# Kernel optimization log

Measured on AMD Instinct MI355X. Metric: run time of the kernel, lower is better.

The kernel has to match this reference:

```python
import jax, jax.numpy as jnp
import numpy as np


def setup_inputs() -> dict:
    key = jax.random.key(0)
    k1, k2 = jax.random.split(key)
    tensor_1 = jax.random.normal(k1, (8192, 256), dtype=jnp.float32)
    tensor_2 = jax.random.normal(k2, (16384, 256), dtype=jnp.float32)
    return {"tensor_1": tensor_1, "tensor_2": tensor_2}


def reference(tensor_1, tensor_2):
    # L2-normalize along the feature dim (matches torch .norm(dim=-1), no eps)
    n1 = tensor_1 / jnp.linalg.norm(tensor_1, axis=-1, keepdims=True)  # [N, d]
    n2 = tensor_2 / jnp.linalg.norm(tensor_2, axis=-1, keepdims=True)  # [M, d]
    cos_sim = jnp.einsum("nd,md->nm", n1, n2)  # [N, M] cosine similarity
    top3, _ = jax.lax.top_k(cos_sim, 3)        # [N, 3]
    return top3.mean(axis=-1)                  # [N]
```

## Files before the change

### kernel.cpp

```cpp
#include <hip/hip_runtime.h>
#include <hip/hip_bf16.h>
#include <stdint.h>

#define N1 8192
#define N2 16384
#define DIM 256
#define NSPLIT 16
#define BM 128
#define BN 128
#define BK 128
#define COLS_PER_SPLIT (N2 / NSPLIT)
#define NT_PER_SPLIT (COLS_PER_SPLIT / BN)
#define NPART (NSPLIT * 2)

typedef short v8s  __attribute__((ext_vector_type(8)));
typedef float f32x4 __attribute__((ext_vector_type(4)));

#define GLD16(g, l)                                                                         \
  __builtin_amdgcn_global_load_lds((const __attribute__((address_space(1))) uint32_t*)(g),  \
                                   (__attribute__((address_space(3))) uint32_t*)(l), 16, 0, 0)

__device__ __forceinline__ void top3_insert(float v, float& t0, float& t1, float& t2) {
    float nt1 = __builtin_amdgcn_fmed3f(v, t0, t1);
    float nt2 = __builtin_amdgcn_fmed3f(v, t1, t2);
    t0 = fmaxf(t0, v);
    t1 = nt1;
    t2 = nt2;
}

__global__ __launch_bounds__(256) void normalize_kernel(
        const float* __restrict__ inA, const float* __restrict__ inB,
        __hip_bfloat16* __restrict__ outA, __hip_bfloat16* __restrict__ outB) {
    const int gw   = blockIdx.x * 4 + (threadIdx.x >> 6);
    const int lane = threadIdx.x & 63;
    const float* in;
    __hip_bfloat16* out;
    int row;
    if (gw < N1) { in = inA; out = outA; row = gw; }
    else         { in = inB; out = outB; row = gw - N1; }
    const float4 v = *(const float4*)(in + (size_t)row * DIM + lane * 4);
    float s = v.x * v.x + v.y * v.y + v.z * v.z + v.w * v.w;
    #pragma unroll
    for (int off = 32; off; off >>= 1) s += __shfl_xor(s, off, 64);
    const float inv = 1.0f / sqrtf(s);
    __hip_bfloat16 o[4];
    o[0] = __float2bfloat16(v.x * inv);
    o[1] = __float2bfloat16(v.y * inv);
    o[2] = __float2bfloat16(v.z * inv);
    o[3] = __float2bfloat16(v.w * inv);
    *(uint2*)(out + (size_t)row * DIM + lane * 4) = *(uint2*)o;
}

__global__ __launch_bounds__(256, 2) void gemm_top3_kernel(
        const __hip_bfloat16* __restrict__ A, const __hip_bfloat16* __restrict__ B,
        float* __restrict__ partial) {
    __shared__ char smem[32768 + 32768];
    char* tileA = smem;
    char* tileB = smem + 32768;

    const int tid  = threadIdx.x;
    const int wave = tid >> 6;
    const int lane = tid & 63;
    const int lo   = lane & 15;
    const int quad = lane >> 4;
    const int rb    = blockIdx.x >> 4;
    const int split = blockIdx.x & 15;
    const int row0 = rb * BM;
    const int C0   = split * COLS_PER_SPLIT;
    const int wr = (wave >> 1) * 64;
    const int wc = (wave & 1) * 64;

    const int lr  = lane >> 4;
    const int s16 = lane & 15;

    const char* Agbase = (const char*)A + ((size_t)(row0 + wave * 32 + lr)) * 512;
    const char* Bgbase = (const char*)B + ((size_t)(C0   + wave * 32 + lr)) * 512;
    char* AldsBase = tileA + wave * 32 * 256;
    char* BldsBase = tileB + wave * 32 * 256;

    int aoff[4], boff[4];
    #pragma unroll
    for (int ks = 0; ks < 4; ks++) {
        const int swz = ((ks * 4 + quad) ^ lo) * 16;
        aoff[ks] = (wr + lo) * 256 + swz;
        boff[ks] = (wc + lo) * 256 + swz;
    }

    float t0[16], t1[16], t2[16];
    #pragma unroll
    for (int i = 0; i < 16; i++) { t0[i] = -1e30f; t1[i] = -1e30f; t2[i] = -1e30f; }

    for (int nt = 0; nt < NT_PER_SPLIT; ++nt) {
        f32x4 acc[4][4];
        #pragma unroll
        for (int kk = 0; kk < 2; kk++) {
            __syncthreads();
            #pragma unroll
            for (int j = 0; j < 8; j++) {
                const int sxj = (s16 ^ ((j * 4 + lr) & 15)) * 16;
                GLD16(Agbase + (size_t)j * 2048 + kk * 256 + sxj, AldsBase + j * 1024);
                GLD16(Bgbase + (size_t)nt * 65536 + (size_t)j * 2048 + kk * 256 + sxj,
                      BldsBase + j * 1024);
            }
            __syncthreads();
            #pragma unroll
            for (int ks = 0; ks < 4; ks++) {
                v8s af[4];
                #pragma unroll
                for (int rt = 0; rt < 4; rt++)
                    af[rt] = *(const v8s*)(tileA + aoff[ks] + rt * 4096);
                #pragma unroll
                for (int ct = 0; ct < 4; ct++) {
                    v8s bf = *(const v8s*)(tileB + boff[ks] + ct * 4096);
                    #pragma unroll
                    for (int rt = 0; rt < 4; rt++) {
                        if (kk == 0 && ks == 0)
                            acc[rt][ct] = __builtin_amdgcn_mfma_f32_16x16x32_bf16(
                                af[rt], bf, (f32x4){0.f, 0.f, 0.f, 0.f}, 0, 0, 0);
                        else
                            acc[rt][ct] = __builtin_amdgcn_mfma_f32_16x16x32_bf16(
                                af[rt], bf, acc[rt][ct], 0, 0, 0);
                    }
                }
            }
        }
        #pragma unroll
        for (int rt = 0; rt < 4; rt++)
            #pragma unroll
            for (int r = 0; r < 4; r++) {
                const int i = rt * 4 + r;
                #pragma unroll
                for (int ct = 0; ct < 4; ct++)
                    top3_insert(acc[rt][ct][r], t0[i], t1[i], t2[i]);
            }
    }

    #pragma unroll
    for (int step = 1; step < 16; step <<= 1) {
        #pragma unroll
        for (int i = 0; i < 16; i++) {
            float b0 = __shfl_xor(t0[i], step, 64);
            float b1 = __shfl_xor(t1[i], step, 64);
            float b2 = __shfl_xor(t2[i], step, 64);
            top3_insert(b0, t0[i], t1[i], t2[i]);
            top3_insert(b1, t0[i], t1[i], t2[i]);
            top3_insert(b2, t0[i], t1[i], t2[i]);
        }
    }

    if (lo == 0) {
        #pragma unroll
        for (int rt = 0; rt < 4; rt++)
            #pragma unroll
            for (int r = 0; r < 4; r++) {
                const int i = rt * 4 + r;
                const int row = row0 + wr + rt * 16 + quad * 4 + r;
                float* p = partial + ((size_t)row * NPART + (split * 2 + (wave & 1))) * 3;
                p[0] = t0[i]; p[1] = t1[i]; p[2] = t2[i];
            }
    }
}

__global__ __launch_bounds__(256) void merge_kernel(
        const float* __restrict__ partial, float* __restrict__ out) {
    const int row = blockIdx.x * 256 + threadIdx.x;
    if (row >= N1) return;
    const float* p = partial + (size_t)row * NPART * 3;
    float t0 = -1e30f, t1 = -1e30f, t2 = -1e30f;
    #pragma unroll
    for (int i = 0; i < NPART * 3; i++) top3_insert(p[i], t0, t1, t2);
    out[row] = (t0 + t1 + t2) * (1.0f / 3.0f);
}

extern "C" void kernel_launch(void* const* d_in, const int* in_sizes, int n_in,
                              void* d_out, int out_size, void* d_ws, size_t ws_size,
                              hipStream_t stream) {
    const float* tA = (const float*)d_in[0];
    const float* tB = (const float*)d_in[1];
    float* out = (float*)d_out;

    __hip_bfloat16* An = (__hip_bfloat16*)d_ws;
    __hip_bfloat16* Bn = An + (size_t)N1 * DIM;
    float* partial = (float*)(Bn + (size_t)N2 * DIM);

    normalize_kernel<<<(N1 + N2) / 4, 256, 0, stream>>>(tA, tB, An, Bn);
    gemm_top3_kernel<<<(N1 / BM) * NSPLIT, 256, 0, stream>>>(An, Bn, partial);
    merge_kernel<<<N1 / 256, 256, 0, stream>>>(partial, out);
}
```

Measured before the change: 153.9 us.

## Double-buffer LDS tiles with BK=64 to overlap global loads with MFMA

```diff
diff --git a/kernel.cpp b/kernel.cpp
--- a/kernel.cpp
+++ b/kernel.cpp
@@ -8,7 +8,7 @@
 #define NSPLIT 16
 #define BM 128
 #define BN 128
-#define BK 128
+#define BK 64
 #define COLS_PER_SPLIT (N2 / NSPLIT)
 #define NT_PER_SPLIT (COLS_PER_SPLIT / BN)
 #define NPART (NSPLIT * 2)
@@ -51,12 +51,19 @@
     *(uint2*)(out + (size_t)row * DIM + lane * 4) = *(uint2*)o;
 }
 
+__device__ __forceinline__ void stage8(const char* ag, const char* bg,
+                                       char* al, char* bl) {
+    #pragma unroll
+    for (int j = 0; j < 4; ++j) {
+        GLD16(ag + (size_t)j * 4096, al + j * 1024);
+        GLD16(bg + (size_t)j * 4096, bl + j * 1024);
+    }
+}
+
 __global__ __launch_bounds__(256, 2) void gemm_top3_kernel(
         const __hip_bfloat16* __restrict__ A, const __hip_bfloat16* __restrict__ B,
         float* __restrict__ partial) {
-    __shared__ char smem[32768 + 32768];
-    char* tileA = smem;
-    char* tileB = smem + 32768;
+    __shared__ char smem[2 * 32768];
 
     const int tid  = threadIdx.x;
     const int wave = tid >> 6;
@@ -70,48 +77,57 @@
     const int wr = (wave >> 1) * 64;
     const int wc = (wave & 1) * 64;
 
-    const int lr  = lane >> 4;
-    const int s16 = lane & 15;
-
-    const char* Agbase = (const char*)A + ((size_t)(row0 + wave * 32 + lr)) * 512;
-    const char* Bgbase = (const char*)B + ((size_t)(C0   + wave * 32 + lr)) * 512;
-    char* AldsBase = tileA + wave * 32 * 256;
-    char* BldsBase = tileB + wave * 32 * 256;
-
-    int aoff[4], boff[4];
-    #pragma unroll
-    for (int ks = 0; ks < 4; ks++) {
-        const int swz = ((ks * 4 + quad) ^ lo) * 16;
-        aoff[ks] = (wr + lo) * 256 + swz;
-        boff[ks] = (wc + lo) * 256 + swz;
+    const int srow   = lane >> 3;
+    const int schunk = (lane & 7) ^ srow;
+    const size_t gl_off = (size_t)srow * 512 + (size_t)schunk * 16;
+
+    const char* Ag = (const char*)A + ((size_t)(row0 + wave * 32)) * 512 + gl_off;
+    const char* Bg = (const char*)B + ((size_t)(C0   + wave * 32)) * 512 + gl_off;
+    char* AldsW = smem + wave * 4096;
+    char* BldsW = smem + 16384 + wave * 4096;
+
+    int aoff[2], boff[2];
+    #pragma unroll
+    for (int ks = 0; ks < 2; ++ks) {
+        const int swz = ((ks * 4 + quad) ^ (lo & 7)) * 16;
+        aoff[ks] = (wr + lo) * 128 + swz;
+        boff[ks] = 16384 + (wc + lo) * 128 + swz;
     }
 
     float t0[16], t1[16], t2[16];
     #pragma unroll
     for (int i = 0; i < 16; i++) { t0[i] = -1e30f; t1[i] = -1e30f; t2[i] = -1e30f; }
+
+    stage8(Ag, Bg, AldsW, BldsW);
 
     for (int nt = 0; nt < NT_PER_SPLIT; ++nt) {
         f32x4 acc[4][4];
         #pragma unroll
-        for (int kk = 0; kk < 2; kk++) {
-            __syncthreads();
+        for (int kk = 0; kk < 4; ++kk) {
+            const int cur = kk & 1;
+            if ((kk < 3) || (nt < NT_PER_SPLIT - 1)) {
+                const int nt2 = (kk == 3) ? nt + 1 : nt;
+                const int kk2 = (kk + 1) & 3;
+                stage8(Ag + kk2 * 128,
+                       Bg + (size_t)nt2 * 65536 + kk2 * 128,
+                       AldsW + (cur ^ 1) * 32768, BldsW + (cur ^ 1) * 32768);
+                asm volatile("s_waitcnt vmcnt(8)" ::: "memory");
+            } else {
+                asm volatile("s_waitcnt vmcnt(0)" ::: "memory");
+            }
+            __builtin_amdgcn_s_barrier();
+            __builtin_amdgcn_sched_barrier(0);
+
+            const char* base = smem + cur * 32768;
             #pragma unroll
-            for (int j = 0; j < 8; j++) {
-                const int sxj = (s16 ^ ((j * 4 + lr) & 15)) * 16;
-                GLD16(Agbase + (size_t)j * 2048 + kk * 256 + sxj, AldsBase + j * 1024);
-                GLD16(Bgbase + (size_t)nt * 65536 + (size_t)j * 2048 + kk * 256 + sxj,
-                      BldsBase + j * 1024);
-            }
-            __syncthreads();
-            #pragma unroll
-            for (int ks = 0; ks < 4; ks++) {
+            for (int ks = 0; ks < 2; ++ks) {
                 v8s af[4];
                 #pragma unroll
                 for (int rt = 0; rt < 4; rt++)
-                    af[rt] = *(const v8s*)(tileA + aoff[ks] + rt * 4096);
+                    af[rt] = *(const v8s*)(base + aoff[ks] + rt * 2048);
                 #pragma unroll
                 for (int ct = 0; ct < 4; ct++) {
-                    v8s bf = *(const v8s*)(tileB + boff[ks] + ct * 4096);
+                    v8s bf = *(const v8s*)(base + boff[ks] + ct * 2048);
                     #pragma unroll
                     for (int rt = 0; rt < 4; rt++) {
                         if (kk == 0 && ks == 0)
@@ -123,6 +139,9 @@
                     }
                 }
             }
+            asm volatile("s_waitcnt lgkmcnt(0)" ::: "memory");
+            __builtin_amdgcn_sched_barrier(0);
+            __builtin_amdgcn_s_barrier();
         }
         #pragma unroll
         for (int rt = 0; rt < 4; rt++)
```

Result: slower. 169.3 us (+10.0%).

## Restructure GEMM-top3 into 512-thread blocks with multi-stage async LDS pipeline

Applied to the files above, without the earlier changes.

```diff
diff --git a/kernel.cpp b/kernel.cpp
--- a/kernel.cpp
+++ b/kernel.cpp
@@ -5,13 +5,10 @@
 #define N1 8192
 #define N2 16384
 #define DIM 256
-#define NSPLIT 16
 #define BM 128
-#define BN 128
-#define BK 128
-#define COLS_PER_SPLIT (N2 / NSPLIT)
-#define NT_PER_SPLIT (COLS_PER_SPLIT / BN)
-#define NPART (NSPLIT * 2)
+#define NTILES 16
+#define CBLK 4
+#define NPART CBLK
 
 typedef short v8s  __attribute__((ext_vector_type(8)));
 typedef float f32x4 __attribute__((ext_vector_type(4)));
@@ -51,113 +48,157 @@
     *(uint2*)(out + (size_t)row * DIM + lane * 4) = *(uint2*)o;
 }
 
-__global__ __launch_bounds__(256, 2) void gemm_top3_kernel(
+__device__ __forceinline__ void stage_half(const char* src_rows, int kk, char* lds_slot,
+                                           int wave, int rbase, int sc16) {
+    GLD16(src_rows + (size_t)rbase * 512 + kk * 128 + sc16, lds_slot + wave * 1024);
+    GLD16(src_rows + (size_t)(rbase + 64) * 512 + kk * 128 + sc16,
+          lds_slot + (8 + wave) * 1024);
+}
+
+__global__ __launch_bounds__(512, 2) void gemm_top3_kernel(
         const __hip_bfloat16* __restrict__ A, const __hip_bfloat16* __restrict__ B,
         float* __restrict__ partial) {
-    __shared__ char smem[32768 + 32768];
-    char* tileA = smem;
-    char* tileB = smem + 32768;
+    __shared__ char smem[114688];
 
     const int tid  = threadIdx.x;
     const int wave = tid >> 6;
     const int lane = tid & 63;
     const int lo   = lane & 15;
     const int quad = lane >> 4;
-    const int rb    = blockIdx.x >> 4;
-    const int split = blockIdx.x & 15;
+    const int m    = wave >> 2;
+    const int n    = wave & 3;
+    const int rb   = blockIdx.x >> 2;
+    const int cb   = blockIdx.x & 3;
     const int row0 = rb * BM;
-    const int C0   = split * COLS_PER_SPLIT;
-    const int wr = (wave >> 1) * 64;
-    const int wc = (wave & 1) * 64;
-
-    const int lr  = lane >> 4;
-    const int s16 = lane & 15;
-
-    const char* Agbase = (const char*)A + ((size_t)(row0 + wave * 32 + lr)) * 512;
-    const char* Bgbase = (const char*)B + ((size_t)(C0   + wave * 32 + lr)) * 512;
-    char* AldsBase = tileA + wave * 32 * 256;
-    char* BldsBase = tileB + wave * 32 * 256;
-
-    int aoff[4], boff[4];
-    #pragma unroll
-    for (int ks = 0; ks < 4; ks++) {
-        const int swz = ((ks * 4 + quad) ^ lo) * 16;
-        aoff[ks] = (wr + lo) * 256 + swz;
-        boff[ks] = (wc + lo) * 256 + swz;
-    }
-
+
+    const int rbase = wave * 8 + (lane >> 3);
+    const int sc16  = ((lane & 7) ^ ((lane >> 3) & 7)) << 4;
+    const char* Ab = (const char*)A + (size_t)row0 * 512;
+    const char* Bb = (const char*)B + (size_t)cb * 4096 * 512;
+
+    const int swz[2] = { (quad ^ (lo & 7)) << 4, ((4 + quad) ^ (lo & 7)) << 4 };
+
+    f32x4 acc[4][4];
+    #pragma unroll
+    for (int i = 0; i < 4; ++i)
+        #pragma unroll
+        for (int j = 0; j < 4; ++j) acc[i][j] = (f32x4){0.f, 0.f, 0.f, 0.f};
     float t0[16], t1[16], t2[16];
     #pragma unroll
-    for (int i = 0; i < 16; i++) { t0[i] = -1e30f; t1[i] = -1e30f; t2[i] = -1e30f; }
-
-    for (int nt = 0; nt < NT_PER_SPLIT; ++nt) {
-        f32x4 acc[4][4];
-        #pragma unroll
-        for (int kk = 0; kk < 2; kk++) {
-            __syncthreads();
+    for (int i = 0; i < 16; ++i) { t0[i] = -1e30f; t1[i] = -1e30f; t2[i] = -1e30f; }
+
+    stage_half(Ab, 0, smem, wave, rbase, sc16);
+    stage_half(Bb, 0, smem + 49152, wave, rbase, sc16);
+    stage_half(Bb + 128 * 512, 0, smem + 49152 + 16384, wave, rbase, sc16);
+    stage_half(Ab, 1, smem + 16384, wave, rbase, sc16);
+    stage_half(Bb, 1, smem + 49152 + 32768, wave, rbase, sc16);
+    stage_half(Bb + 128 * 512, 1, smem + 49152 + 49152, wave, rbase, sc16);
+    asm volatile("s_waitcnt vmcnt(6)" ::: "memory");
+    __builtin_amdgcn_s_barrier();
+
+    int am = 0;
+    v8s bf[4][2];
+    for (int nt = 0; nt < NTILES; ++nt) {
+        #pragma unroll
+        for (int P = 0; P < 8; ++P) {
+            const int k = P >> 1, h = P & 1, par = k & 1;
+            int sA = am + k; if (sA >= 3) sA -= 3;
+            v8s af[2][2];
+            const char* ap = smem + sA * 16384 + (m * 64 + h * 32 + lo) * 128;
             #pragma unroll
-            for (int j = 0; j < 8; j++) {
-                const int sxj = (s16 ^ ((j * 4 + lr) & 15)) * 16;
-                GLD16(Agbase + (size_t)j * 2048 + kk * 256 + sxj, AldsBase + j * 1024);
-                GLD16(Bgbase + (size_t)nt * 65536 + (size_t)j * 2048 + kk * 256 + sxj,
-                      BldsBase + j * 1024);
-            }
-            __syncthreads();
+            for (int rt = 0; rt < 2; ++rt)
+                #pragma unroll
+                for (int ks = 0; ks < 2; ++ks)
+                    af[rt][ks] = *(const v8s*)(ap + rt * 2048 + swz[ks]);
+            if (h == 0) {
+                const char* bp = smem + 49152 + par * 32768 + (n >> 1) * 16384
+                               + ((n & 1) * 64 + lo) * 128;
+                #pragma unroll
+                for (int ct = 0; ct < 4; ++ct)
+                    #pragma unroll
+                    for (int ks = 0; ks < 2; ++ks)
+                        bf[ct][ks] = *(const v8s*)(bp + ct * 2048 + swz[ks]);
+            }
+            if (h == 0) {
+                if (!(nt == NTILES - 1 && k >= 2)) {
+                    int s2 = am + k + 2;
+                    if (s2 >= 3) s2 -= 3;
+                    if (s2 >= 3) s2 -= 3;
+                    stage_half(Ab, (k + 2) & 3, smem + s2 * 16384, wave, rbase, sc16);
+                }
+            } else {
+                if (!(nt == NTILES - 1 && k >= 2)) {
+                    const int kb  = (k + 2) & 3;
+                    const char* bsrc = Bb + (size_t)((nt + (k >> 1)) * 256) * 512;
+                    char* bdst = smem + 49152 + par * 32768;
+                    stage_half(bsrc, kb, bdst, wave, rbase, sc16);
+                    stage_half(bsrc + 128 * 512, kb, bdst + 16384, wave, rbase, sc16);
+                }
+            }
+            __builtin_amdgcn_s_barrier();
+            __builtin_amdgcn_s_setprio(1);
             #pragma unroll
-            for (int ks = 0; ks < 4; ks++) {
-                v8s af[4];
-                #pragma unroll
-                for (int rt = 0; rt < 4; rt++)
-                    af[rt] = *(const v8s*)(tileA + aoff[ks] + rt * 4096);
-                #pragma unroll
-                for (int ct = 0; ct < 4; ct++) {
-                    v8s bf = *(const v8s*)(tileB + boff[ks] + ct * 4096);
+            for (int ks = 0; ks < 2; ++ks)
+                #pragma unroll
+                for (int ct = 0; ct < 4; ++ct)
                     #pragma unroll
-                    for (int rt = 0; rt < 4; rt++) {
-                        if (kk == 0 && ks == 0)
-                            acc[rt][ct] = __builtin_amdgcn_mfma_f32_16x16x32_bf16(
-                                af[rt], bf, (f32x4){0.f, 0.f, 0.f, 0.f}, 0, 0, 0);
-                        else
-                            acc[rt][ct] = __builtin_amdgcn_mfma_f32_16x16x32_bf16(
-                                af[rt], bf, acc[rt][ct], 0, 0, 0);
-                    }
-                }
-            }
+                    for (int rt = 0; rt < 2; ++rt)
+                        acc[h * 2 + rt][ct] = __builtin_amdgcn_mfma_f32_16x16x32_bf16(
+                            af[rt][ks], bf[ct][ks], acc[h * 2 + rt][ct], 0, 0, 0);
+            __builtin_amdgcn_s_setprio(0);
+            if (h == 1) {
+                if (nt == NTILES - 1 && P == 5) {
+                    asm volatile("s_waitcnt vmcnt(0)" ::: "memory");
+                } else if (!(nt == NTILES - 1 && P == 7)) {
+                    asm volatile("s_waitcnt vmcnt(6)" ::: "memory");
+                }
+            }
+            __builtin_amdgcn_s_barrier();
         }
         #pragma unroll
-        for (int rt = 0; rt < 4; rt++)
+        for (int i = 0; i < 4; ++i)
             #pragma unroll
-            for (int r = 0; r < 4; r++) {
-                const int i = rt * 4 + r;
-                #pragma unroll
-                for (int ct = 0; ct < 4; ct++)
-                    top3_insert(acc[rt][ct][r], t0[i], t1[i], t2[i]);
-            }
+            for (int r = 0; r < 4; ++r) {
+                const int s = i * 4 + r;
+                #pragma unroll
+                for (int ct = 0; ct < 4; ++ct) {
+                    top3_insert(acc[i][ct][r], t0[s], t1[s], t2[s]);
+                    acc[i][ct][r] = 0.f;
+                }
+            }
+        am = (am == 2) ? 0 : am + 1;
     }
 
     #pragma unroll
     for (int step = 1; step < 16; step <<= 1) {
         #pragma unroll
-        for (int i = 0; i < 16; i++) {
-            float b0 = __shfl_xor(t0[i], step, 64);
-            float b1 = __shfl_xor(t1[i], step, 64);
-            float b2 = __shfl_xor(t2[i], step, 64);
-            top3_insert(b0, t0[i], t1[i], t2[i]);
-            top3_insert(b1, t0[i], t1[i], t2[i]);
-            top3_insert(b2, t0[i], t1[i], t2[i]);
+        for (int s = 0; s < 16; ++s) {
+            float b0 = __shfl_xor(t0[s], step, 64);
+            float b1 = __shfl_xor(t1[s], step, 64);
+            float b2 = __shfl_xor(t2[s], step, 64);
+            top3_insert(b0, t0[s], t1[s], t2[s]);
+            top3_insert(b1, t0[s], t1[s], t2[s]);
+            top3_insert(b2, t0[s], t1[s], t2[s]);
         }
     }
 
+    float* fbuf = (float*)smem;
     if (lo == 0) {
         #pragma unroll
-        for (int rt = 0; rt < 4; rt++)
-            #pragma unroll
-            for (int r = 0; r < 4; r++) {
-                const int i = rt * 4 + r;
-                const int row = row0 + wr + rt * 16 + quad * 4 + r;
-                float* p = partial + ((size_t)row * NPART + (split * 2 + (wave & 1))) * 3;
-                p[0] = t0[i]; p[1] = t1[i]; p[2] = t2[i];
-            }
+        for (int s = 0; s < 16; ++s) {
+            const int row = m * 64 + (s >> 2) * 16 + quad * 4 + (s & 3);
+            float* p = fbuf + row * 12 + n * 3;
+            p[0] = t0[s]; p[1] = t1[s]; p[2] = t2[s];
+        }
+    }
+    __syncthreads();
+    if (tid < BM) {
+        const float* p = fbuf + tid * 12;
+        float u0 = p[0], u1 = p[1], u2 = p[2];
+        #pragma unroll
+        for (int i = 3; i < 12; ++i) top3_insert(p[i], u0, u1, u2);
+        float* o = partial + ((size_t)(row0 + tid) * NPART + cb) * 3;
+        o[0] = u0; o[1] = u1; o[2] = u2;
     }
 }
 
@@ -184,6 +225,6 @@
     float* partial = (float*)(Bn + (size_t)N2 * DIM);
 
     normalize_kernel<<<(N1 + N2) / 4, 256, 0, stream>>>(tA, tB, An, Bn);
-    gemm_top3_kernel<<<(N1 / BM) * NSPLIT, 256, 0, stream>>>(An, Bn, partial);
+    gemm_top3_kernel<<<(N1 / BM) * CBLK, 512, 0, stream>>>(An, Bn, partial);
     merge_kernel<<<N1 / 256, 256, 0, stream>>>(partial, out);
 }
```

New measurement: 150.3 us. 2.4% less time.
